# Performance work log

Measured on AMD Instinct MI355X. Metric: run time of the kernel, lower is better.

## Reference

```python
import jax, jax.numpy as jnp
import numpy as np

N_HEADS = 8
D_EMBED = 1024
D_CROSS = 768
D_HEAD = D_EMBED // N_HEADS


def setup_inputs() -> dict:
    key = jax.random.key(0)
    ks = jax.random.split(key, 10)
    B, SQ, SKV = 8, 4096, 77
    scale_e = 1.0 / np.sqrt(D_EMBED)
    scale_c = 1.0 / np.sqrt(D_CROSS)
    return {
        "x": jax.random.normal(ks[0], (B, SQ, D_EMBED), dtype=jnp.float32),
        "y": jax.random.normal(ks[1], (B, SKV, D_CROSS), dtype=jnp.float32),
        # weights stored as [in, out] so projection is x @ W + b
        "Wq": jax.random.normal(ks[2], (D_EMBED, D_EMBED), dtype=jnp.float32) * scale_e,
        "bq": jnp.zeros((D_EMBED,), dtype=jnp.float32),
        "Wk": jax.random.normal(ks[3], (D_CROSS, D_EMBED), dtype=jnp.float32) * scale_c,
        "bk": jnp.zeros((D_EMBED,), dtype=jnp.float32),
        "Wv": jax.random.normal(ks[4], (D_CROSS, D_EMBED), dtype=jnp.float32) * scale_c,
        "bv": jnp.zeros((D_EMBED,), dtype=jnp.float32),
        "Wo": jax.random.normal(ks[5], (D_EMBED, D_EMBED), dtype=jnp.float32) * scale_e,
        "bo": jnp.zeros((D_EMBED,), dtype=jnp.float32),
    }


def reference(x, y, Wq, bq, Wk, bk, Wv, bv, Wo, bo):
    B, SQ, _ = x.shape
    # projections
    q = x @ Wq + bq                      # [B, SQ, D_EMBED]
    k = y @ Wk + bk                      # [B, SKV, D_EMBED]
    v = y @ Wv + bv                      # [B, SKV, D_EMBED]
    # split heads -> [B, H, S, Dh]
    q = q.reshape(B, SQ, N_HEADS, D_HEAD).transpose(0, 2, 1, 3)
    k = k.reshape(B, -1, N_HEADS, D_HEAD).transpose(0, 2, 1, 3)
    v = v.reshape(B, -1, N_HEADS, D_HEAD).transpose(0, 2, 1, 3)
    # attention: q@k^T / sqrt(d_head), softmax, @v
    scale = 1.0 / jnp.sqrt(jnp.asarray(D_HEAD, dtype=q.dtype))
    weight = jnp.einsum("bhqd,bhkd->bhqk", q, k) * scale  # [B, H, SQ, SKV]
    weight = jax.nn.softmax(weight, axis=-1)
    out = jnp.einsum("bhqk,bhkd->bhqd", weight, v)        # [B, H, SQ, Dh]
    out = out.transpose(0, 2, 1, 3).reshape(B, SQ, D_EMBED)
    return out @ Wo + bo
```

## Files before the change

kernel.cpp:

```cpp
#include <hip/hip_runtime.h>

typedef _Float16 half_t;
typedef _Float16 half8 __attribute__((ext_vector_type(8)));
typedef float f32x4 __attribute__((ext_vector_type(4)));

#define D_EMBED   1024
#define D_CROSS   768
#define N_HEADS   8
#define D_HEAD    128
#define BATCH     8
#define SEQ_Q     4096
#define SEQ_KV    77
#define SKV_PAD   80
#define NKV       (N_HEADS*SKV_PAD)
#define M_Q       (BATCH*SEQ_Q)

#define WS_S     ((size_t)0)
#define WS_WQC   (WS_S    + (size_t)M_Q*NKV*2)
#define WS_WOT   (WS_WQC  + (size_t)D_EMBED*D_EMBED*2)
#define WS_WKVT  (WS_WOT  + (size_t)D_EMBED*D_EMBED*2)
#define WS_YH    (WS_WKVT + (size_t)2*D_EMBED*D_CROSS*2)
#define WS_KV    (WS_YH   + (size_t)BATCH*SKV_PAD*D_CROSS*2)
#define WS_BKV   (WS_KV   + (size_t)BATCH*SKV_PAD*2*D_EMBED*2)
#define WS_BT1   (WS_BKV  + (size_t)2*D_EMBED*4)
#define WS_BT2   (WS_BT1  + (size_t)BATCH*NKV*D_EMBED*2)
#define WS_C1    (WS_BT2  + (size_t)BATCH*D_EMBED*NKV*2)

#define ATTN_SCALE 0.08838834764831845f

__device__ __forceinline__ void gload_lds16(const void* g, void* lds) {
  __builtin_amdgcn_global_load_lds(
      (const __attribute__((address_space(1))) unsigned int*)g,
      (__attribute__((address_space(3))) unsigned int*)lds, 16, 0, 0);
}
__device__ __forceinline__ void BAR() {
  __builtin_amdgcn_s_barrier();
  __builtin_amdgcn_sched_barrier(0);
}

__global__ void cast_f32_f16(const float* __restrict__ src, half_t* __restrict__ dst) {
  int i = blockIdx.x * 256 + threadIdx.x;
  f32x4 a = *(const f32x4*)(src + (size_t)i*8);
  f32x4 b = *(const f32x4*)(src + (size_t)i*8 + 4);
  half8 h;
#pragma unroll
  for (int j = 0; j < 4; ++j) { h[j] = (half_t)a[j]; h[j+4] = (half_t)b[j]; }
  *(half8*)(dst + (size_t)i*8) = h;
}

__global__ void transpose_f32f16(const float* __restrict__ src, half_t* __restrict__ dst,
                                 int K, int N) {
  __shared__ float tile[32][33];
  int n0 = blockIdx.x * 32, k0 = blockIdx.y * 32;
  int tx = threadIdx.x, ty = threadIdx.y;
#pragma unroll
  for (int j = 0; j < 4; ++j)
    tile[ty + j*8][tx] = src[(size_t)(k0 + ty + j*8)*N + n0 + tx];
  __syncthreads();
#pragma unroll
  for (int j = 0; j < 4; ++j)
    dst[(size_t)(n0 + ty + j*8)*K + k0 + tx] = (half_t)tile[tx][ty + j*8];
}

__global__ void convert_pad_y(const float* __restrict__ y, half_t* __restrict__ yh) {
  int idx = blockIdx.x * 256 + threadIdx.x;
  int r = idx / D_CROSS, col = idx - r*D_CROSS;
  int b = r / SKV_PAD, s = r - b*SKV_PAD;
  yh[idx] = (s < SEQ_KV) ? (half_t)y[(size_t)(b*SEQ_KV + s)*D_CROSS + col] : (half_t)0.f;
}

__global__ void concat_bias(const float* __restrict__ bk, const float* __restrict__ bv,
                            float* __restrict__ bkv) {
  int i = blockIdx.x * 256 + threadIdx.x;
  bkv[i] = (i < D_EMBED) ? bk[i] : bv[i - D_EMBED];
}

__global__ __launch_bounds__(256, 3)
void gemm_kv(const half_t* __restrict__ A, const half_t* __restrict__ Bt,
             const float* __restrict__ bias, half_t* __restrict__ C,
             int M, int N, int K) {
  __shared__ half_t As[3][128*32];
  __shared__ half_t Bs[2][128*32];
  const int tid = threadIdx.x;
  const int l = tid & 63, w = tid >> 6;
  const int l4 = l & 15, lh = l >> 4;
  const int bn0 = blockIdx.x * 128, bm0 = blockIdx.y * 128;
  const int wr = w >> 1, wc = w & 1;
  const int rslot = lh << 4;
  f32x4 acc[4][4] = {};
  const int nk = K >> 5;
  const int srow = w*16 + (l >> 2);
  const int scol = (l & 3)*8;

  auto stageB = [&](int kt, int bb) {
    const half_t* g = Bt + (size_t)(bn0 + srow)*K + scol + kt*32;
    gload_lds16(g,                 (char*)Bs[bb] + w*1024);
    gload_lds16(g + (size_t)64*K,  (char*)Bs[bb] + 4096 + w*1024);
  };
  auto stageA = [&](int kt, int bb) {
    const half_t* g = A + (size_t)(bm0 + srow)*K + scol + kt*32;
    gload_lds16(g,                 (char*)As[bb] + w*1024);
    gload_lds16(g + (size_t)64*K,  (char*)As[bb] + 4096 + w*1024);
  };
  auto compute = [&](int ab, int bb) {
    half8 af[4], bf[4];
#pragma unroll
    for (int m = 0; m < 4; ++m)
      af[m] = *(const half8*)((const char*)As[ab] + (size_t)(wr*64 + m*16 + l4)*64 + rslot);
#pragma unroll
    for (int n = 0; n < 4; ++n)
      bf[n] = *(const half8*)((const char*)Bs[bb] + (size_t)(wc*64 + n*16 + l4)*64 + rslot);
#pragma unroll
    for (int m = 0; m < 4; ++m)
#pragma unroll
      for (int n = 0; n < 4; ++n)
        acc[m][n] = __builtin_amdgcn_mfma_f32_16x16x32_f16(af[m], bf[n], acc[m][n], 0, 0, 0);
  };

  stageA(0, 0); stageA(1, 1); stageB(0, 0);
  asm volatile("s_waitcnt vmcnt(0)" ::: "memory");
  BAR();
  int aCur = 0, aP2 = 2;
  for (int t = 0; t < nk; ++t) {
    if (t + 1 < nk) stageB(t + 1, (t + 1) & 1);
    if (t + 2 < nk) stageA(t + 2, aP2);
    compute(aCur, t & 1);
    if (t + 1 < nk) {
      if (t + 2 < nk) { asm volatile("s_waitcnt vmcnt(2)" ::: "memory"); }
      else            { asm volatile("s_waitcnt vmcnt(0)" ::: "memory"); }
      BAR();
    }
    aCur = (aCur == 2) ? 0 : aCur + 1;
    aP2  = (aP2  == 2) ? 0 : aP2  + 1;
  }

  const int cb = bn0 + wc*64, rb = bm0 + wr*64;
#pragma unroll
  for (int n = 0; n < 4; ++n) {
    const int col = cb + n*16 + l4;
    const float bvv = bias[col];
#pragma unroll
    for (int m = 0; m < 4; ++m)
#pragma unroll
      for (int j = 0; j < 4; ++j)
        C[(size_t)(rb + m*16 + lh*4 + j)*N + col] = (half_t)(acc[m][n][j] + bvv);
  }
}

__global__ __launch_bounds__(256, 2)
void w1_build(const half_t* __restrict__ kvb, const half_t* __restrict__ Wqc,
              half_t* __restrict__ Bt1) {
  __shared__ half_t K_lds[80*136];
  const int blk = blockIdx.x;
  const int b = blk >> 3, h = blk & 7;
  const int tid = threadIdx.x;
  const int l = tid & 63, w = tid >> 6;
  const int l4 = l & 15, lh = l >> 4;
  for (int i = tid; i < 80*16; i += 256) {
    int s = i >> 4, d = (i & 15) << 3;
    *(half8*)(K_lds + s*136 + d) =
        *(const half8*)(kvb + (size_t)(b*SKV_PAD + s)*2048 + h*128 + d);
  }
  __syncthreads();
  for (int c = 0; c < 4; ++c) {
    f32x4 acc[5][4] = {};
#pragma unroll
    for (int kt = 0; kt < 4; ++kt) {
      half8 af[5], bf[4];
#pragma unroll
      for (int m = 0; m < 5; ++m)
        af[m] = *(const half8*)(K_lds + (size_t)(m*16 + l4)*136 + kt*32 + lh*8);
#pragma unroll
      for (int n = 0; n < 4; ++n)
        bf[n] = *(const half8*)(Wqc + (size_t)(w*256 + c*64 + n*16 + l4)*1024 + h*128 + kt*32 + lh*8);
#pragma unroll
      for (int m = 0; m < 5; ++m)
#pragma unroll
        for (int n = 0; n < 4; ++n)
          acc[m][n] = __builtin_amdgcn_mfma_f32_16x16x32_f16(af[m], bf[n], acc[m][n], 0, 0, 0);
    }
#pragma unroll
    for (int n = 0; n < 4; ++n) {
      const int colk = w*256 + c*64 + n*16 + l4;
#pragma unroll
      for (int m = 0; m < 5; ++m)
#pragma unroll
        for (int j = 0; j < 4; ++j) {
          const int srow = m*16 + lh*4 + j;
          size_t byte = (((size_t)(b*NKV + h*SKV_PAD + srow))*1024 + colk)*2;
          byte ^= ((size_t)((srow >> 1) & 3)) << 4;
          *(half_t*)((char*)Bt1 + byte) = (half_t)(acc[m][n][j]*ATTN_SCALE);
        }
    }
  }
}

__global__ __launch_bounds__(256, 2)
void w2_build(const half_t* __restrict__ kvb, const half_t* __restrict__ Wot,
              half_t* __restrict__ Bt2) {
  __shared__ half_t V_lds[80*136];
  const int blk = blockIdx.x;
  const int b = blk >> 3, h = blk & 7;
  const int tid = threadIdx.x;
  const int l = tid & 63, w = tid >> 6;
  const int l4 = l & 15, lh = l >> 4;
  for (int i = tid; i < 80*16; i += 256) {
    int s = i >> 4, d = (i & 15) << 3;
    *(half8*)(V_lds + s*136 + d) =
        *(const half8*)(kvb + (size_t)(b*SKV_PAD + s)*2048 + 1024 + h*128 + d);
  }
  __syncthreads();
  for (int c = 0; c < 4; ++c) {
    f32x4 acc[4][5] = {};
#pragma unroll
    for (int kt = 0; kt < 4; ++kt) {
      half8 af[4], bf[5];
#pragma unroll
      for (int m = 0; m < 4; ++m)
        af[m] = *(const half8*)(Wot + (size_t)(w*256 + c*64 + m*16 + l4)*1024 + h*128 + kt*32 + lh*8);
#pragma unroll
      for (int n = 0; n < 5; ++n)
        bf[n] = *(const half8*)(V_lds + (size_t)(n*16 + l4)*136 + kt*32 + lh*8);
#pragma unroll
      for (int m = 0; m < 4; ++m)
#pragma unroll
        for (int n = 0; n < 5; ++n)
          acc[m][n] = __builtin_amdgcn_mfma_f32_16x16x32_f16(af[m], bf[n], acc[m][n], 0, 0, 0);
    }
#pragma unroll
    for (int m = 0; m < 4; ++m) {
#pragma unroll
      for (int j = 0; j < 4; ++j) {
        const int nrow = w*256 + c*64 + m*16 + lh*4 + j;
        const size_t rowbase = ((size_t)(b*1024 + nrow))*1280;
#pragma unroll
        for (int n = 0; n < 5; ++n) {
          const int cc = h*80 + n*16 + l4;
          size_t byte = rowbase + (size_t)(cc >> 6)*128
                        + ((size_t)(((cc >> 3) & 7) ^ (nrow & 7)) << 4) + ((cc & 7) << 1);
          *(half_t*)((char*)Bt2 + byte) = (half_t)acc[m][n][j];
        }
      }
    }
  }
}

__global__ void c1_build(const half_t* __restrict__ kvb, const float* __restrict__ bq,
                         float* __restrict__ c1) {
  int idx = blockIdx.x * 256 + threadIdx.x;
  int b = idx / NKV, n = idx - b*NKV;
  int h = n / SKV_PAD, s = n - h*SKV_PAD;
  const half_t* kp = kvb + (size_t)(b*SKV_PAD + s)*2048 + h*128;
  float acc = 0.f;
#pragma unroll 8
  for (int d = 0; d < 128; ++d) acc += bq[h*128 + d] * (float)kp[d];
  c1[idx] = acc * ATTN_SCALE;
}

template<int NBX>
__global__ __launch_bounds__(256, 3)
void gemm_s(const float* __restrict__ Av, const half_t* __restrict__ BtAll,
            const float* __restrict__ biasAll, half_t* __restrict__ Cv,
            int M, int N, int K) {
  __shared__ half_t As[2][128*32];
  __shared__ half_t Bs[3][128*32];
  const int tid = threadIdx.x;
  const int l  = tid & 63;
  const int w  = tid >> 6;
  const int l4 = l & 15, lh = l >> 4;

  const int chunk = (int)gridDim.x >> 3;
  const int sb = blockIdx.x;
  const int lin = (sb & 7)*chunk + (sb >> 3);
  const int bx = lin % NBX;
  const int by = lin / NBX;
  const int b  = by >> 5;
  const half_t* Bt  = BtAll  + (size_t)b*NKV*1024;
  const float* bias = biasAll + (size_t)b*NKV;

  const int bn0 = bx * 128;
  const int bm0 = by * 128;
  const int wr = w >> 1, wc = w & 1;
  const int aslot = lh << 4;
  const int bslot = (lh ^ ((l4 >> 1) & 3)) << 4;

  f32x4 acc[4][4] = {};
  const int nk = K >> 5;
  const int srow = w*16 + (l >> 2);
  const int scol = (l & 3)*8;

  auto stageB = [&](int kt, int bb) {
    const half_t* g = Bt + (size_t)(bn0 + srow)*K + scol + kt*32;
    gload_lds16(g,                (char*)Bs[bb] + w*1024);
    gload_lds16(g + (size_t)64*K, (char*)Bs[bb] + 4096 + w*1024);
  };

  f32x4 L0, L1, L2, L3;
  const int arow = tid >> 2;
  const int ac0  = (tid & 3) * 8;
  const int wslot = (tid & 3) << 4;
  auto aload = [&](int kt) {
    const float* g0 = Av + (size_t)(bm0 + arow)*K + kt*32 + ac0;
    const float* g1 = Av + (size_t)(bm0 + 64 + arow)*K + kt*32 + ac0;
    L0 = *(const f32x4*)g0; L1 = *(const f32x4*)(g0 + 4);
    L2 = *(const f32x4*)g1; L3 = *(const f32x4*)(g1 + 4);
  };
  auto awrite = [&](int bb) {
    half8 h0, h1;
#pragma unroll
    for (int j = 0; j < 4; ++j) { h0[j] = (half_t)L0[j]; h0[j+4] = (half_t)L1[j]; }
#pragma unroll
    for (int j = 0; j < 4; ++j) { h1[j] = (half_t)L2[j]; h1[j+4] = (half_t)L3[j]; }
    *(half8*)((char*)As[bb] + (size_t)arow*64 + wslot)        = h0;
    *(half8*)((char*)As[bb] + (size_t)(64 + arow)*64 + wslot) = h1;
  };

  auto compute = [&](int ab, int bb) {
    half8 af[4], bf[4];
#pragma unroll
    for (int m = 0; m < 4; ++m)
      af[m] = *(const half8*)((const char*)As[ab] + (size_t)(wr*64 + m*16 + l4)*64 + aslot);
#pragma unroll
    for (int n = 0; n < 4; ++n)
      bf[n] = *(const half8*)((const char*)Bs[bb] + (size_t)(wc*64 + n*16 + l4)*64 + bslot);
#pragma unroll
    for (int m = 0; m < 4; ++m)
#pragma unroll
      for (int n = 0; n < 4; ++n)
        acc[m][n] = __builtin_amdgcn_mfma_f32_16x16x32_f16(af[m], bf[n], acc[m][n], 0, 0, 0);
  };

  aload(0); stageB(0, 0); stageB(1, 1);
  awrite(0);
  asm volatile("s_waitcnt vmcnt(2) lgkmcnt(0)" ::: "memory");
  BAR();
  int bCur = 0, bP2 = 2;
  for (int t = 0; t < nk; ++t) {
    if (t + 1 < nk) aload(t + 1);
    if (t + 2 < nk) stageB(t + 2, bP2);
    compute(t & 1, bCur);
    if (t + 1 < nk) {
      awrite((t + 1) & 1);
      asm volatile("s_waitcnt lgkmcnt(0)" ::: "memory");
      BAR();
    }
    bCur = (bCur == 2) ? 0 : bCur + 1;
    bP2  = (bP2  == 2) ? 0 : bP2  + 1;
  }

  const int c_base = bn0 + wc*64;
  const int r_base = bm0 + wr*64;
#pragma unroll
  for (int n = 0; n < 4; ++n) {
    const int col = c_base + n*16 + l4;
    const float bvv = bias[col];
#pragma unroll
    for (int m = 0; m < 4; ++m) {
#pragma unroll
      for (int j = 0; j < 4; ++j) {
        const int row = r_base + m*16 + lh*4 + j;
        const float v = acc[m][n][j] + bvv;
        size_t byte = (size_t)row*1280 + (size_t)(col >> 6)*128
                      + ((size_t)(((col >> 3) & 7) ^ (row & 7)) << 4) + ((col & 7) << 1);
        *(half_t*)((char*)Cv + byte) = (half_t)v;
      }
    }
  }
}

__global__ __launch_bounds__(256, 4)
void softmax_inplace(half_t* __restrict__ S) {
  const int gid = blockIdx.x * 256 + threadIdx.x;
  const int row = gid >> 3, h = gid & 7;
  const int key = row & 7;
  char* base = (char*)S + (size_t)row*1280;
  size_t off[10];
  half8 v[10];
#pragma unroll
  for (int i = 0; i < 10; ++i) {
    const int ls = h*10 + i;
    off[i] = (size_t)(ls >> 3)*128 + ((size_t)((ls & 7) ^ key) << 4);
    v[i] = *(const half8*)(base + off[i]);
  }
  float mx = -1e30f;
#pragma unroll
  for (int i = 0; i < 10; ++i)
#pragma unroll
    for (int j = 0; j < 8; ++j)
      if (i*8 + j < SEQ_KV) mx = fmaxf(mx, (float)v[i][j]);
  float sm = 0.f;
#pragma unroll
  for (int i = 0; i < 10; ++i) {
    half8 t = v[i];
#pragma unroll
    for (int j = 0; j < 8; ++j) {
      float e = (i*8 + j < SEQ_KV) ? __expf((float)t[j] - mx) : 0.f;
      sm += e; t[j] = (half_t)e;
    }
    v[i] = t;
  }
  const float inv = 1.f / sm;
#pragma unroll
  for (int i = 0; i < 10; ++i) {
    half8 t = v[i];
#pragma unroll
    for (int j = 0; j < 8; ++j) t[j] = (half_t)((float)t[j] * inv);
    *(half8*)(base + off[i]) = t;
  }
}

#define PH8(Q, ABASE, PRE, TAIL)                                                                     \
  {                                                                                                  \
    half8 a00 = *(const half8*)((ABASE) + (size_t)(arow0 + (2*(Q)  )*16)*128 + ak0);                 \
    half8 a01 = *(const half8*)((ABASE) + (size_t)(arow0 + (2*(Q)  )*16)*128 + ak1);                 \
    half8 a10 = *(const half8*)((ABASE) + (size_t)(arow0 + (2*(Q)+1)*16)*128 + ak0);                 \
    half8 a11 = *(const half8*)((ABASE) + (size_t)(arow0 + (2*(Q)+1)*16)*128 + ak1);                 \
    PRE;                                                                                             \
    __builtin_amdgcn_s_barrier();                                                                    \
    asm volatile("s_waitcnt lgkmcnt(0)" ::: "memory");                                               \
    __builtin_amdgcn_sched_barrier(0);                                                               \
    __builtin_amdgcn_s_setprio(1);                                                                   \
    _Pragma("unroll")                                                                                \
    for (int ni = 0; ni < 4; ++ni) {                                                                 \
      acc[2*(Q)  ][ni] = __builtin_amdgcn_mfma_f32_16x16x32_f16(a00, bf[ni][0], acc[2*(Q)  ][ni],0,0,0); \
      acc[2*(Q)  ][ni] = __builtin_amdgcn_mfma_f32_16x16x32_f16(a01, bf[ni][1], acc[2*(Q)  ][ni],0,0,0); \
      acc[2*(Q)+1][ni] = __builtin_amdgcn_mfma_f32_16x16x32_f16(a10, bf[ni][0], acc[2*(Q)+1][ni],0,0,0); \
      acc[2*(Q)+1][ni] = __builtin_amdgcn_mfma_f32_16x16x32_f16(a11, bf[ni][1], acc[2*(Q)+1][ni],0,0,0); \
    }                                                                                                \
    __builtin_amdgcn_s_setprio(0);                                                                   \
    TAIL;                                                                                            \
    __builtin_amdgcn_s_barrier();                                                                    \
    __builtin_amdgcn_sched_barrier(0);                                                               \
  }

__global__ __launch_bounds__(512, 1)
void gemm8p_out(const half_t* __restrict__ Sa, const half_t* __restrict__ Bt2,
                const float* __restrict__ bo, float* __restrict__ out) {
  __shared__ half_t AbS[2*256*64];
  __shared__ half_t BbS[2*256*64];
  char* ABp = (char*)AbS;
  char* BBp = (char*)BbS;
  const int tid = threadIdx.x;
  const int l = tid & 63, w = tid >> 6;
  const int l4 = l & 15, lh = l >> 4;
  const int lin = ((int)blockIdx.x & 7)*64 + ((int)blockIdx.x >> 3);
  const int bx = lin & 3, by = lin >> 2;
  const int bm0 = by << 8, bn0 = bx << 8;
  const half_t* Bt = Bt2 + (size_t)(by >> 4)*1024*640;
  const int wr = w >> 2, wc = w & 3;
  const int ak0 = ((lh    ) ^ (l4 & 7)) << 4;
  const int ak1 = ((lh + 4) ^ (l4 & 7)) << 4;
  const int arow0 = wr*128 + l4;
  const int brow0 = wc*64 + l4;
  f32x4 acc[8][4] = {};
  half8 bf[4][2];

  auto stA = [&](int kt, int db, int hf) {
#pragma unroll
    for (int r = 0; r < 2; ++r) {
      const int id = tid + r*512;
      gload_lds16((const char*)Sa + (size_t)(bm0 + hf*128 + (id >> 3))*1280 + (size_t)kt*128 + (id & 7)*16,
                  ABp + db*32768 + hf*16384 + r*8192 + w*1024);
    }
  };
  auto stB = [&](int kt, int db, int hf) {
#pragma unroll
    for (int r = 0; r < 2; ++r) {
      const int id = tid + r*512;
      gload_lds16((const char*)Bt + (size_t)(bn0 + hf*128 + (id >> 3))*1280 + (size_t)kt*128 + (id & 7)*16,
                  BBp + db*32768 + hf*16384 + r*8192 + w*1024);
    }
  };
  auto rdB = [&](const char* base) {
#pragma unroll
    for (int ni = 0; ni < 4; ++ni) {
      bf[ni][0] = *(const half8*)(base + (size_t)(brow0 + ni*16)*128 + ak0);
      bf[ni][1] = *(const half8*)(base + (size_t)(brow0 + ni*16)*128 + ak1);
    }
  };

  stA(0, 0, 0); stA(0, 0, 1); stB(0, 0, 0); stB(0, 0, 1); stB(1, 1, 0); stB(1, 1, 1);
  asm volatile("s_waitcnt vmcnt(4)" ::: "memory");
  __builtin_amdgcn_sched_barrier(0);
  __builtin_amdgcn_s_barrier();

  const char* A0 = ABp;            const char* A1 = ABp + 32768;
  const char* B0 = BBp;            const char* B1 = BBp + 32768;

  for (int u = 0; u < 5; ++u) {
    const int kt0 = 2*u, kt1 = 2*u + 1;
    const bool nx = (u < 4);
    PH8(0, A0, { rdB(B0); stA(kt1, 1, 0); stA(kt1, 1, 1); }, {});
    PH8(1, A0, { if (nx) stB(kt0 + 2, 0, 0); }, {});
    PH8(2, A0, { if (nx) stB(kt0 + 2, 0, 1); }, {});
    PH8(3, A0, {}, {
      if (nx) { asm volatile("s_waitcnt vmcnt(4)" ::: "memory"); }
      else    { asm volatile("s_waitcnt vmcnt(0)" ::: "memory"); }
      __builtin_amdgcn_sched_barrier(0);
    });
    PH8(0, A1, { rdB(B1); if (nx) stA(kt0 + 2, 0, 0); }, {});
    PH8(1, A1, { if (nx) stA(kt0 + 2, 0, 1); }, {});
    PH8(2, A1, { if (nx) stB(kt1 + 2, 1, 0); }, {});
    PH8(3, A1, { if (nx) stB(kt1 + 2, 1, 1); }, {
      if (nx) {
        asm volatile("s_waitcnt vmcnt(4)" ::: "memory");
        __builtin_amdgcn_sched_barrier(0);
      }
    });
  }

#pragma unroll
  for (int ni = 0; ni < 4; ++ni) {
    const int col = bn0 + wc*64 + ni*16 + l4;
    const float bvv = bo[col];
#pragma unroll
    for (int mi = 0; mi < 8; ++mi)
#pragma unroll
      for (int j = 0; j < 4; ++j) {
        const int row = bm0 + wr*128 + mi*16 + lh*4 + j;
        out[(size_t)row*1024 + col] = acc[mi][ni][j] + bvv;
      }
  }
}

extern "C" void kernel_launch(void* const* d_in, const int* in_sizes, int n_in,
                              void* d_out, int out_size, void* d_ws, size_t ws_size,
                              hipStream_t stream) {
  (void)in_sizes; (void)n_in; (void)out_size; (void)ws_size;
  const float* x  = (const float*)d_in[0];
  const float* y  = (const float*)d_in[1];
  const float* Wq = (const float*)d_in[2];
  const float* bq = (const float*)d_in[3];
  const float* Wk = (const float*)d_in[4];
  const float* bk = (const float*)d_in[5];
  const float* Wv = (const float*)d_in[6];
  const float* bv = (const float*)d_in[7];
  const float* Wo = (const float*)d_in[8];
  const float* bo = (const float*)d_in[9];

  char* ws = (char*)d_ws;
  half_t* S    = (half_t*)(ws + WS_S);
  half_t* Wqc  = (half_t*)(ws + WS_WQC);
  half_t* Wot  = (half_t*)(ws + WS_WOT);
  half_t* Wkvt = (half_t*)(ws + WS_WKVT);
  half_t* yh   = (half_t*)(ws + WS_YH);
  half_t* kvb  = (half_t*)(ws + WS_KV);
  float*  bkv  = (float*)(ws + WS_BKV);
  half_t* Bt1  = (half_t*)(ws + WS_BT1);
  half_t* Bt2  = (half_t*)(ws + WS_BT2);
  float*  c1   = (float*)(ws + WS_C1);

  dim3 tb(32, 8);
  cast_f32_f16<<<512, 256, 0, stream>>>(Wq, Wqc);
  transpose_f32f16<<<dim3(32, 32), tb, 0, stream>>>(Wo, Wot, 1024, 1024);
  transpose_f32f16<<<dim3(32, 24), tb, 0, stream>>>(Wk, Wkvt, 768, 1024);
  transpose_f32f16<<<dim3(32, 24), tb, 0, stream>>>(Wv, Wkvt + (size_t)1024*768, 768, 1024);
  convert_pad_y<<<BATCH*SKV_PAD*D_CROSS/256, 256, 0, stream>>>(y, yh);
  concat_bias<<<2*D_EMBED/256, 256, 0, stream>>>(bk, bv, bkv);

  gemm_kv<<<dim3(16, 5), 256, 0, stream>>>(yh, Wkvt, bkv, kvb, BATCH*SKV_PAD, 2048, 768);

  c1_build<<<BATCH*NKV/256, 256, 0, stream>>>(kvb, bq, c1);
  w1_build<<<BATCH*N_HEADS, 256, 0, stream>>>(kvb, Wqc, Bt1);
  w2_build<<<BATCH*N_HEADS, 256, 0, stream>>>(kvb, Wot, Bt2);

  gemm_s<5><<<1280, 256, 0, stream>>>(x, Bt1, c1, S, M_Q, NKV, 1024);

  softmax_inplace<<<M_Q*N_HEADS/256, 256, 0, stream>>>(S);

  gemm8p_out<<<512, 512, 0, stream>>>(S, Bt2, bo, (float*)d_out);
}
```

Before: 290.9 us.

## Replace score GEMM with 256x256-tile 8-wave pipelined kernel and padded Bt1

Swaps the 128x128 score GEMM (x @ folded Wq·K^T) for a 512-thread kernel using 256x256 tiles and the phased PH8 MFMA schedule already used by the output GEMM. To get there, Bt1 is padded to 768 columns per batch and stored in an XOR-swizzled 64-wide K layout, and a new kernel zeroes the pad rows. The larger tiles increase reuse of each loaded operand and cut the number of blocks. The cost is about 17% wasted MFMA work on padded columns, an extra small launch, and fewer blocks (384), which may leave parts of the GPU underused.

```diff
diff --git a/kernel.cpp b/kernel.cpp
--- a/kernel.cpp
+++ b/kernel.cpp
@@ -13,6 +13,7 @@
 #define SEQ_KV    77
 #define SKV_PAD   80
 #define NKV       (N_HEADS*SKV_PAD)
+#define NKV_PAD   768
 #define M_Q       (BATCH*SEQ_Q)
 
 #define WS_S     ((size_t)0)
@@ -23,7 +24,7 @@
 #define WS_KV    (WS_YH   + (size_t)BATCH*SKV_PAD*D_CROSS*2)
 #define WS_BKV   (WS_KV   + (size_t)BATCH*SKV_PAD*2*D_EMBED*2)
 #define WS_BT1   (WS_BKV  + (size_t)2*D_EMBED*4)
-#define WS_BT2   (WS_BT1  + (size_t)BATCH*NKV*D_EMBED*2)
+#define WS_BT2   (WS_BT1  + (size_t)BATCH*NKV_PAD*D_EMBED*2)
 #define WS_C1    (WS_BT2  + (size_t)BATCH*D_EMBED*NKV*2)
 
 #define ATTN_SCALE 0.08838834764831845f
@@ -186,13 +187,26 @@
       for (int m = 0; m < 5; ++m)
 #pragma unroll
         for (int j = 0; j < 4; ++j) {
-          const int srow = m*16 + lh*4 + j;
-          size_t byte = (((size_t)(b*NKV + h*SKV_PAD + srow))*1024 + colk)*2;
-          byte ^= ((size_t)((srow >> 1) & 3)) << 4;
+          const int r = h*SKV_PAD + m*16 + lh*4 + j;
+          size_t byte = ((size_t)(b*NKV_PAD + r))*2048 + (size_t)(colk >> 6)*128
+                        + ((size_t)(((colk >> 3) & 7) ^ (r & 7)) << 4) + ((colk & 7) << 1);
           *(half_t*)((char*)Bt1 + byte) = (half_t)(acc[m][n][j]*ATTN_SCALE);
         }
     }
   }
+}
+
+__global__ void zero_bt1_pad(half_t* __restrict__ Bt1) {
+  int idx = blockIdx.x * 256 + threadIdx.x;
+  int flat = idx * 8;
+  int b = flat >> 17;
+  int rem = flat & 131071;
+  int row = NKV + (rem >> 10);
+  int col = rem & 1023;
+  size_t byte = ((size_t)(b*NKV_PAD + row))*2048 + (size_t)(col >> 6)*128
+                + ((size_t)(((col >> 3) & 7) ^ (row & 7)) << 4);
+  half8 z = {};
+  *(half8*)((char*)Bt1 + byte) = z;
 }
 
 __global__ __launch_bounds__(256, 2)
@@ -255,158 +269,6 @@
 #pragma unroll 8
   for (int d = 0; d < 128; ++d) acc += bq[h*128 + d] * (float)kp[d];
   c1[idx] = acc * ATTN_SCALE;
-}
-
-template<int NBX>
-__global__ __launch_bounds__(256, 3)
-void gemm_s(const float* __restrict__ Av, const half_t* __restrict__ BtAll,
-            const float* __restrict__ biasAll, half_t* __restrict__ Cv,
-            int M, int N, int K) {
-  __shared__ half_t As[2][128*32];
-  __shared__ half_t Bs[3][128*32];
-  const int tid = threadIdx.x;
-  const int l  = tid & 63;
-  const int w  = tid >> 6;
-  const int l4 = l & 15, lh = l >> 4;
-
-  const int chunk = (int)gridDim.x >> 3;
-  const int sb = blockIdx.x;
-  const int lin = (sb & 7)*chunk + (sb >> 3);
-  const int bx = lin % NBX;
-  const int by = lin / NBX;
-  const int b  = by >> 5;
-  const half_t* Bt  = BtAll  + (size_t)b*NKV*1024;
-  const float* bias = biasAll + (size_t)b*NKV;
-
-  const int bn0 = bx * 128;
-  const int bm0 = by * 128;
-  const int wr = w >> 1, wc = w & 1;
-  const int aslot = lh << 4;
-  const int bslot = (lh ^ ((l4 >> 1) & 3)) << 4;
-
-  f32x4 acc[4][4] = {};
-  const int nk = K >> 5;
-  const int srow = w*16 + (l >> 2);
-  const int scol = (l & 3)*8;
-
-  auto stageB = [&](int kt, int bb) {
-    const half_t* g = Bt + (size_t)(bn0 + srow)*K + scol + kt*32;
-    gload_lds16(g,                (char*)Bs[bb] + w*1024);
-    gload_lds16(g + (size_t)64*K, (char*)Bs[bb] + 4096 + w*1024);
-  };
-
-  f32x4 L0, L1, L2, L3;
-  const int arow = tid >> 2;
-  const int ac0  = (tid & 3) * 8;
-  const int wslot = (tid & 3) << 4;
-  auto aload = [&](int kt) {
-    const float* g0 = Av + (size_t)(bm0 + arow)*K + kt*32 + ac0;
-    const float* g1 = Av + (size_t)(bm0 + 64 + arow)*K + kt*32 + ac0;
-    L0 = *(const f32x4*)g0; L1 = *(const f32x4*)(g0 + 4);
-    L2 = *(const f32x4*)g1; L3 = *(const f32x4*)(g1 + 4);
-  };
-  auto awrite = [&](int bb) {
-    half8 h0, h1;
-#pragma unroll
-    for (int j = 0; j < 4; ++j) { h0[j] = (half_t)L0[j]; h0[j+4] = (half_t)L1[j]; }
-#pragma unroll
-    for (int j = 0; j < 4; ++j) { h1[j] = (half_t)L2[j]; h1[j+4] = (half_t)L3[j]; }
-    *(half8*)((char*)As[bb] + (size_t)arow*64 + wslot)        = h0;
-    *(half8*)((char*)As[bb] + (size_t)(64 + arow)*64 + wslot) = h1;
-  };
-
-  auto compute = [&](int ab, int bb) {
-    half8 af[4], bf[4];
-#pragma unroll
-    for (int m = 0; m < 4; ++m)
-      af[m] = *(const half8*)((const char*)As[ab] + (size_t)(wr*64 + m*16 + l4)*64 + aslot);
-#pragma unroll
-    for (int n = 0; n < 4; ++n)
-      bf[n] = *(const half8*)((const char*)Bs[bb] + (size_t)(wc*64 + n*16 + l4)*64 + bslot);
-#pragma unroll
-    for (int m = 0; m < 4; ++m)
-#pragma unroll
-      for (int n = 0; n < 4; ++n)
-        acc[m][n] = __builtin_amdgcn_mfma_f32_16x16x32_f16(af[m], bf[n], acc[m][n], 0, 0, 0);
-  };
-
-  aload(0); stageB(0, 0); stageB(1, 1);
-  awrite(0);
-  asm volatile("s_waitcnt vmcnt(2) lgkmcnt(0)" ::: "memory");
-  BAR();
-  int bCur = 0, bP2 = 2;
-  for (int t = 0; t < nk; ++t) {
-    if (t + 1 < nk) aload(t + 1);
-    if (t + 2 < nk) stageB(t + 2, bP2);
-    compute(t & 1, bCur);
-    if (t + 1 < nk) {
-      awrite((t + 1) & 1);
-      asm volatile("s_waitcnt lgkmcnt(0)" ::: "memory");
-      BAR();
-    }
-    bCur = (bCur == 2) ? 0 : bCur + 1;
-    bP2  = (bP2  == 2) ? 0 : bP2  + 1;
-  }
-
-  const int c_base = bn0 + wc*64;
-  const int r_base = bm0 + wr*64;
-#pragma unroll
-  for (int n = 0; n < 4; ++n) {
-    const int col = c_base + n*16 + l4;
-    const float bvv = bias[col];
-#pragma unroll
-    for (int m = 0; m < 4; ++m) {
-#pragma unroll
-      for (int j = 0; j < 4; ++j) {
-        const int row = r_base + m*16 + lh*4 + j;
-        const float v = acc[m][n][j] + bvv;
-        size_t byte = (size_t)row*1280 + (size_t)(col >> 6)*128
-                      + ((size_t)(((col >> 3) & 7) ^ (row & 7)) << 4) + ((col & 7) << 1);
-        *(half_t*)((char*)Cv + byte) = (half_t)v;
-      }
-    }
-  }
-}
-
-__global__ __launch_bounds__(256, 4)
-void softmax_inplace(half_t* __restrict__ S) {
-  const int gid = blockIdx.x * 256 + threadIdx.x;
-  const int row = gid >> 3, h = gid & 7;
-  const int key = row & 7;
-  char* base = (char*)S + (size_t)row*1280;
-  size_t off[10];
-  half8 v[10];
-#pragma unroll
-  for (int i = 0; i < 10; ++i) {
-    const int ls = h*10 + i;
-    off[i] = (size_t)(ls >> 3)*128 + ((size_t)((ls & 7) ^ key) << 4);
-    v[i] = *(const half8*)(base + off[i]);
-  }
-  float mx = -1e30f;
-#pragma unroll
-  for (int i = 0; i < 10; ++i)
-#pragma unroll
-    for (int j = 0; j < 8; ++j)
-      if (i*8 + j < SEQ_KV) mx = fmaxf(mx, (float)v[i][j]);
-  float sm = 0.f;
-#pragma unroll
-  for (int i = 0; i < 10; ++i) {
-    half8 t = v[i];
-#pragma unroll
-    for (int j = 0; j < 8; ++j) {
-      float e = (i*8 + j < SEQ_KV) ? __expf((float)t[j] - mx) : 0.f;
-      sm += e; t[j] = (half_t)e;
-    }
-    v[i] = t;
-  }
-  const float inv = 1.f / sm;
-#pragma unroll
-  for (int i = 0; i < 10; ++i) {
-    half8 t = v[i];
-#pragma unroll
-    for (int j = 0; j < 8; ++j) t[j] = (half_t)((float)t[j] * inv);
-    *(half8*)(base + off[i]) = t;
-  }
 }
 
 #define PH8(Q, ABASE, PRE, TAIL)                                                                     \
@@ -434,6 +296,149 @@
   }
 
 __global__ __launch_bounds__(512, 1)
+void gemm8p_s(const float* __restrict__ X, const half_t* __restrict__ Bt1,
+              const float* __restrict__ c1, half_t* __restrict__ S) {
+  __shared__ half_t AbS[2*256*64];
+  __shared__ half_t BbS[2*256*64];
+  char* ABp = (char*)AbS;
+  char* BBp = (char*)BbS;
+  const int tid = threadIdx.x;
+  const int l = tid & 63, w = tid >> 6;
+  const int l4 = l & 15, lh = l >> 4;
+  const int lin = ((int)blockIdx.x & 7)*48 + ((int)blockIdx.x >> 3);
+  const int bx = lin % 3, by = lin / 3;
+  const int bm0 = by << 8, bn0 = bx << 8;
+  const int batch = by >> 4;
+  const half_t* Bt = Bt1 + (size_t)batch*NKV_PAD*1024;
+  const float* c1b = c1 + (size_t)batch*NKV;
+  const int wr = w >> 2, wc = w & 3;
+  const int ak0 = ((lh    ) ^ (l4 & 7)) << 4;
+  const int ak1 = ((lh + 4) ^ (l4 & 7)) << 4;
+  const int arow0 = wr*128 + l4;
+  const int brow0 = wc*64 + l4;
+  f32x4 acc[8][4] = {};
+  half8 bf[4][2];
+
+  f32x4 L[8];
+  const int arow = tid >> 1;
+  const int acb  = (tid & 1) * 32;
+  const int akey = arow & 7;
+  auto aload = [&](int kt) {
+    const float* g = X + (size_t)(bm0 + arow)*1024 + kt*64 + acb;
+#pragma unroll
+    for (int j = 0; j < 8; ++j) L[j] = *(const f32x4*)(g + j*4);
+  };
+  auto awrite = [&](int db) {
+    char* base = ABp + db*32768 + (size_t)arow*128;
+#pragma unroll
+    for (int j = 0; j < 4; ++j) {
+      half8 h;
+#pragma unroll
+      for (int e = 0; e < 4; ++e) { h[e] = (half_t)L[2*j][e]; h[e+4] = (half_t)L[2*j+1][e]; }
+      *(half8*)(base + ((((tid & 1)*4 + j) ^ akey) << 4)) = h;
+    }
+  };
+  auto stB = [&](int kt, int db, int hf) {
+#pragma unroll
+    for (int r = 0; r < 2; ++r) {
+      const int id = tid + r*512;
+      gload_lds16((const char*)Bt + (size_t)(bn0 + hf*128 + (id >> 3))*2048 + (size_t)kt*128 + (id & 7)*16,
+                  BBp + db*32768 + hf*16384 + r*8192 + w*1024);
+    }
+  };
+  auto rdB = [&](const char* base) {
+#pragma unroll
+    for (int ni = 0; ni < 4; ++ni) {
+      bf[ni][0] = *(const half8*)(base + (size_t)(brow0 + ni*16)*128 + ak0);
+      bf[ni][1] = *(const half8*)(base + (size_t)(brow0 + ni*16)*128 + ak1);
+    }
+  };
+
+  aload(0); awrite(0);
+  stB(0, 0, 0); stB(0, 0, 1); stB(1, 1, 0); stB(1, 1, 1);
+  asm volatile("s_waitcnt vmcnt(4) lgkmcnt(0)" ::: "memory");
+  __builtin_amdgcn_sched_barrier(0);
+  __builtin_amdgcn_s_barrier();
+
+  const char* A0 = ABp;            const char* A1 = ABp + 32768;
+  const char* B0 = BBp;            const char* B1 = BBp + 32768;
+
+  for (int u = 0; u < 8; ++u) {
+    const int kt0 = 2*u, kt1 = 2*u + 1;
+    const bool nx = (u < 7);
+    PH8(0, A0, { rdB(B0); aload(kt1); }, {});
+    PH8(1, A0, { if (nx) stB(kt0 + 2, 0, 0); }, {});
+    PH8(2, A0, { if (nx) stB(kt0 + 2, 0, 1); awrite(1); }, {});
+    PH8(3, A0, {}, {});
+    PH8(0, A1, { rdB(B1); if (nx) aload(kt0 + 2); }, {});
+    PH8(1, A1, { if (nx) stB(kt1 + 2, 1, 0); }, {});
+    PH8(2, A1, { if (nx) { stB(kt1 + 2, 1, 1); awrite(0); } }, {});
+    PH8(3, A1, {}, {
+      if (!nx) { asm volatile("s_waitcnt vmcnt(0)" ::: "memory"); }
+    });
+  }
+
+#pragma unroll
+  for (int ni = 0; ni < 4; ++ni) {
+    const int col = bn0 + wc*64 + ni*16 + l4;
+    if (col < NKV) {
+      const float bvv = c1b[col];
+#pragma unroll
+      for (int mi = 0; mi < 8; ++mi)
+#pragma unroll
+        for (int j = 0; j < 4; ++j) {
+          const int row = bm0 + wr*128 + mi*16 + lh*4 + j;
+          const float v = acc[mi][ni][j] + bvv;
+          size_t byte = (size_t)row*1280 + (size_t)(col >> 6)*128
+                        + ((size_t)(((col >> 3) & 7) ^ (row & 7)) << 4) + ((col & 7) << 1);
+          *(half_t*)((char*)S + byte) = (half_t)v;
+        }
+    }
+  }
+}
+
+__global__ __launch_bounds__(256, 4)
+void softmax_inplace(half_t* __restrict__ S) {
+  const int gid = blockIdx.x * 256 + threadIdx.x;
+  const int row = gid >> 3, h = gid & 7;
+  const int key = row & 7;
+  char* base = (char*)S + (size_t)row*1280;
+  size_t off[10];
+  half8 v[10];
+#pragma unroll
+  for (int i = 0; i < 10; ++i) {
+    const int ls = h*10 + i;
+    off[i] = (size_t)(ls >> 3)*128 + ((size_t)((ls & 7) ^ key) << 4);
+    v[i] = *(const half8*)(base + off[i]);
+  }
+  float mx = -1e30f;
+#pragma unroll
+  for (int i = 0; i < 10; ++i)
+#pragma unroll
+    for (int j = 0; j < 8; ++j)
+      if (i*8 + j < SEQ_KV) mx = fmaxf(mx, (float)v[i][j]);
+  float sm = 0.f;
+#pragma unroll
+  for (int i = 0; i < 10; ++i) {
+    half8 t = v[i];
+#pragma unroll
+    for (int j = 0; j < 8; ++j) {
+      float e = (i*8 + j < SEQ_KV) ? __expf((float)t[j] - mx) : 0.f;
+      sm += e; t[j] = (half_t)e;
+    }
+    v[i] = t;
+  }
+  const float inv = 1.f / sm;
+#pragma unroll
+  for (int i = 0; i < 10; ++i) {
+    half8 t = v[i];
+#pragma unroll
+    for (int j = 0; j < 8; ++j) t[j] = (half_t)((float)t[j] * inv);
+    *(half8*)(base + off[i]) = t;
+  }
+}
+
+__global__ __launch_bounds__(512, 1)
 void gemm8p_out(const half_t* __restrict__ Sa, const half_t* __restrict__ Bt2,
                 const float* __restrict__ bo, float* __restrict__ out) {
   __shared__ half_t AbS[2*256*64];
@@ -562,9 +567,10 @@
 
   c1_build<<<BATCH*NKV/256, 256, 0, stream>>>(kvb, bq, c1);
   w1_build<<<BATCH*N_HEADS, 256, 0, stream>>>(kvb, Wqc, Bt1);
+  zero_bt1_pad<<<512, 256, 0, stream>>>(Bt1);
   w2_build<<<BATCH*N_HEADS, 256, 0, stream>>>(kvb, Wot, Bt2);
 
-  gemm_s<5><<<1280, 256, 0, stream>>>(x, Bt1, c1, S, M_Q, NKV, 1024);
+  gemm8p_s<<<384, 512, 0, stream>>>(x, Bt1, c1, S);
 
   softmax_inplace<<<M_Q*N_HEADS/256, 256, 0, stream>>>(S);
 
```

Measured after the change: 338.4 us. 1.16x slower.
